# Kernel optimization log

Measured on AMD Instinct MI355X. Metric: run time of the kernel, lower is better.

## Reference

```python
import jax, jax.numpy as jnp
import numpy as np

EPS = 1e-06
SOUND_SPEED = 343.0
SUBBAND_EDGES = [500.0, 2000.0, 8000.0]
IS_SOUND_IDX = 0
RHO_IDX = 1
NUM_CANDIDATES = 64


def setup_inputs() -> dict:
    key = jax.random.key(0)
    ks = jax.random.split(key, 6)
    B, T, F, S, D = 16, 2048, 1025, 4, NUM_CANDIDATES
    phase = jax.random.normal(ks[0], (B, 1, T, F), dtype=jnp.float32)
    comb = jax.random.normal(ks[1], (B, 2, T, F), dtype=jnp.float32)
    scalar = jax.random.normal(ks[2], (B, T, S), dtype=jnp.float32)
    scalar_observed_mask = jax.random.uniform(ks[3], (B, T, S), dtype=jnp.float32)
    scalar_reliable_mask = jax.random.uniform(ks[4], (B, T, S), dtype=jnp.float32)
    stpacc = jax.random.normal(ks[5], (B, 1, T, D), dtype=jnp.float32)
    # STFT bin centers up to 24 kHz
    frequencies_hz = (jnp.arange(F, dtype=jnp.float32) * (24000.0 / (F - 1)))
    spacing_grid_hz = jnp.linspace(50.0, 1000.0, D, dtype=jnp.float32)
    return {
        'phase': phase, 'comb': comb, 'scalar': scalar,
        'scalar_observed_mask': scalar_observed_mask,
        'scalar_reliable_mask': scalar_reliable_mask,
        'stpacc': stpacc, 'frequencies_hz': frequencies_hz,
        'spacing_grid_hz': spacing_grid_hz,
    }


def _periodicity_basis(freq, spacing):
    # [D, F]: raised-cosine comb pattern for each candidate spacing
    pattern = 0.5 * (1.0 + jnp.cos(2.0 * np.pi * (freq[None, :] / jnp.maximum(spacing[:, None], 1e-06))))
    return pattern / jnp.maximum(pattern.mean(axis=-1, keepdims=True), EPS)


def _subband_masks(freq):
    # static boundaries: [min(f)] + edges + [max(f)+1]; all bands nonempty for this grid
    bounds = [jnp.min(freq)] + [jnp.float32(e) for e in SUBBAND_EDGES] + [jnp.max(freq) + 1.0]
    masks = [((freq >= lo) & (freq < hi)).astype(freq.dtype) for lo, hi in zip(bounds[:-1], bounds[1:])]
    return jnp.stack(masks, axis=0)  # [S_band, F]


def reference(phase, comb, scalar, scalar_observed_mask, scalar_reliable_mask,
              stpacc, frequencies_hz, spacing_grid_hz):
    freq = frequencies_hz.astype(phase.dtype)
    log_mag = phase[:, 0, :, :]                 # [B,T,F]
    smooth_d1 = comb[:, 0, :, :]
    abs_d1 = jnp.abs(comb[:, 1, :, :])
    log_mag_centered = log_mag - jnp.mean(log_mag, axis=-1, keepdims=True)
    trough = jax.nn.relu(-log_mag_centered)
    d1_strength = jax.nn.relu(abs_d1) + 0.25 * jax.nn.relu(jnp.abs(smooth_d1))
    trough = trough * (1.0 + d1_strength)
    trough = trough / jnp.maximum(jnp.mean(trough, axis=-1, keepdims=True), EPS)

    basis = _periodicity_basis(freq, spacing_grid_hz.astype(phase.dtype))  # [D,F]
    D, F = basis.shape
    periodic_score = jnp.einsum('btf,df->btd', trough, basis) / float(F)

    channels = [periodic_score]
    bands = _subband_masks(freq)                           # [Sb,F]
    denom = jnp.maximum(jnp.sum(bands, axis=-1), 1.0)      # [Sb]
    masked_basis = basis[None, :, :] * bands[:, None, :]   # [Sb,D,F]
    band_scores = jnp.einsum('btf,sdf->bstd', trough, masked_basis) / denom[None, :, None, None]
    channels += [band_scores[:, s] for s in range(bands.shape[0])]

    # stpacc projection (last dim already == D, no interpolation needed)
    stp = jax.nn.relu(stpacc[:, 0, :, :])
    stp = stp / jnp.maximum(jnp.mean(stp, axis=-1, keepdims=True), EPS)
    channels.append(stp)

    B, T = trough.shape[0], trough.shape[1]
    obs_quality = jnp.broadcast_to(jnp.mean(scalar_observed_mask, axis=-1, keepdims=True), (B, T, D))
    rel_quality = jnp.broadcast_to(jnp.mean(scalar_reliable_mask, axis=-1, keepdims=True), (B, T, D))
    channels.append(obs_quality)
    channels.append(rel_quality)

    is_sound = jnp.broadcast_to(jnp.clip(scalar[:, :, IS_SOUND_IDX:IS_SOUND_IDX + 1], 0.0, 1.0), (B, T, D))
    channels.append(is_sound)
    rho = jnp.broadcast_to(jnp.abs(jnp.clip(scalar[:, :, RHO_IDX:RHO_IDX + 1], -1.0, 1.0)), (B, T, D))
    channels.append(rho)

    raw_likelihood_seq = jnp.stack(channels, axis=-1)      # [B,T,D,10]
    raw_distance_logits_seq = jnp.mean(raw_likelihood_seq, axis=-1) * (0.5 + 0.5 * is_sound)

    distance_grid_cm = (100.0 * SOUND_SPEED) / (2.0 * jnp.maximum(spacing_grid_hz, 1e-06))
    return (raw_likelihood_seq, raw_distance_logits_seq,
            spacing_grid_hz.astype(phase.dtype), distance_grid_cm.astype(phase.dtype))
```

## Files before the change

### kernel.cpp

```cpp
#include <hip/hip_runtime.h>
#include <hip/hip_fp16.h>
#include <math.h>

#define Bn 16
#define Tn 2048
#define Fn 1025
#define KP 1056
#define KROW 1064
#define Dn 64
#define EPSF 1e-6f

typedef __attribute__((ext_vector_type(8))) _Float16 f16x8;
typedef __attribute__((ext_vector_type(4))) _Float16 f16x4;
typedef __attribute__((ext_vector_type(4))) float f32x4;

__device__ inline float waveReduceSum(float v) {
#pragma unroll
  for (int off = 32; off > 0; off >>= 1) v += __shfl_xor(v, off, 64);
  return v;
}

__global__ __launch_bounds__(256) void prep_kernel(
    const float* __restrict__ freq, const float* __restrict__ spacing,
    _Float16* __restrict__ basisT, float* __restrict__ out2, float* __restrict__ out3) {
  __shared__ float wsum[4];
  const int d = blockIdx.x;
  const int tid = threadIdx.x;
  const float sp = fmaxf(spacing[d], 1e-6f);

  float pv[5];
  float lsum = 0.f;
#pragma unroll
  for (int it = 0; it < 5; ++it) {
    int f = tid + 256 * it;
    float p = 0.f;
    if (f < Fn) {
      double arg = 6.2831853071795864769 * (double)(freq[f] / sp);
      p = 0.5f * (1.0f + (float)cos(arg));
      lsum += p;
    }
    pv[it] = p;
  }
  float s = waveReduceSum(lsum);
  if ((tid & 63) == 0) wsum[tid >> 6] = s;
  __syncthreads();
  float inv = 1.0f / fmaxf((wsum[0] + wsum[1] + wsum[2] + wsum[3]) * (1.0f / 1025.0f), EPSF);

#pragma unroll
  for (int it = 0; it < 5; ++it) {
    int f = tid + 256 * it;
    if (f < KP) basisT[(size_t)d * KP + f] = (_Float16)(pv[it] * inv);
  }
  if (tid == 0) {
    out2[d] = spacing[d];
    out3[d] = 17150.0f / sp;
  }
}

__global__ __launch_bounds__(256) void fused_kernel(
    const float* __restrict__ phase, const float* __restrict__ comb,
    const _Float16* __restrict__ basisT,
    const float* __restrict__ scalar, const float* __restrict__ obs_m,
    const float* __restrict__ rel_m, const float* __restrict__ stpacc,
    float* __restrict__ out0, float* __restrict__ out1) {
  __shared__ _Float16 uLDS[16 * KROW];

  const int lane = threadIdx.x & 63;
  const int w = __builtin_amdgcn_readfirstlane(threadIdx.x >> 6);
  const int row0 = blockIdx.x * 16;

#pragma unroll 1
  for (int k4 = 0; k4 < 4; ++k4) {
    const int rl = w * 4 + k4;
    const int row = row0 + rl;
    const int b = row >> 11;
    const int t = row & 2047;

    const float* prow  = phase + (size_t)row * Fn;
    const float* c0row = comb + ((size_t)(b * 2 + 0) * Tn + t) * Fn;
    const float* c1row = comb + ((size_t)(b * 2 + 1) * Tn + t) * Fn;

    float4 pv[5], c0v[5], c1v[5];
#pragma unroll
    for (int it = 0; it < 5; ++it) {
      const int i = lane + 64 * it;
      if (i < 256) {
        pv[it]  = *(const float4*)(prow  + 4 * i);
        c0v[it] = *(const float4*)(c0row + 4 * i);
        c1v[it] = *(const float4*)(c1row + 4 * i);
      } else if (i == 256) {
        pv[it]  = make_float4(prow[1024],  0.f, 0.f, 0.f);
        c0v[it] = make_float4(c0row[1024], 0.f, 0.f, 0.f);
        c1v[it] = make_float4(c1row[1024], 0.f, 0.f, 0.f);
      } else {
        pv[it]  = make_float4(0.f, 0.f, 0.f, 0.f);
        c0v[it] = make_float4(0.f, 0.f, 0.f, 0.f);
        c1v[it] = make_float4(0.f, 0.f, 0.f, 0.f);
      }
    }

    float s = 0.f;
#pragma unroll
    for (int it = 0; it < 5; ++it)
      s += pv[it].x + pv[it].y + pv[it].z + pv[it].w;
    s = waveReduceSum(s);
    const float mean_lm = s * (1.0f / 1025.0f);

    float4 uv[5];
    float su = 0.f;
#pragma unroll
    for (int it = 0; it < 5; ++it) {
      const int i = lane + 64 * it;
      float4 u;
      const float* pf = (const float*)&pv[it];
      const float* q0 = (const float*)&c0v[it];
      const float* q1 = (const float*)&c1v[it];
      float* uf = (float*)&u;
#pragma unroll
      for (int c2 = 0; c2 < 4; ++c2) {
        float tr = fmaxf(mean_lm - pf[c2], 0.f);
        float d1 = fabsf(q1[c2]) + 0.25f * fabsf(q0[c2]);
        uf[c2] = tr * (1.f + d1);
      }
      if (i > 256) { u.x = 0.f; u.y = 0.f; u.z = 0.f; u.w = 0.f; }
      else if (i == 256) { u.y = 0.f; u.z = 0.f; u.w = 0.f; }
      uv[it] = u;
      su += u.x + u.y + u.z + u.w;
    }
    su = waveReduceSum(su);
    const float rs = 1.0f / fmaxf(su * (1.0f / 1025.0f), EPSF);

    _Float16* urow = uLDS + (size_t)rl * KROW;
#pragma unroll
    for (int it = 0; it < 5; ++it) {
      const int i = lane + 64 * it;
      if (i < 264) {
        const float* uf = (const float*)&uv[it];
        f16x4 hv;
#pragma unroll
        for (int c2 = 0; c2 < 4; ++c2) hv[c2] = (_Float16)(uf[c2] * rs);
        *(f16x4*)(urow + 4 * i) = hv;
      }
    }
  }
  __syncthreads();

  const int m16 = lane & 15;
  const int kg = lane >> 4;
  const int nh = w & 1;
  const int kh = w >> 1;
  const int d0 = nh * 32 + m16;

  const _Float16* ALp = uLDS + (size_t)m16 * KROW + kg * 8;
  const _Float16* B0 = basisT + (size_t)d0 * KP + kg * 8;
  const _Float16* B1 = basisT + (size_t)(d0 + 16) * KP + kg * 8;

  f32x4 acc0 = {0.f, 0.f, 0.f, 0.f};
  f32x4 acc1 = {0.f, 0.f, 0.f, 0.f};
  f32x4 s0a = acc0, s0b = acc0, s1a = acc0, s1b = acc0, s2a = acc0, s2b = acc0;

  auto loadA = [&](int kt) { return *(const f16x8*)(ALp + kt * 32); };
  auto tileA = [&](int kt, f16x8 a) {
    f16x8 b0 = *(const f16x8*)(B0 + kt * 32);
    f16x8 b1 = *(const f16x8*)(B1 + kt * 32);
    acc0 = __builtin_amdgcn_mfma_f32_16x16x32_f16(a, b0, acc0, 0, 0, 0);
    acc1 = __builtin_amdgcn_mfma_f32_16x16x32_f16(a, b1, acc1, 0, 0, 0);
  };
  auto boundary = [&](int kt, int KB, f32x4& sa, f32x4& sb) {
    f16x8 a = loadA(kt);
    const int kb = kt * 32 + kg * 8;
    f16x8 alo, ahi;
#pragma unroll
    for (int j = 0; j < 8; ++j) {
      bool lo = (kb + j) < KB;
      alo[j] = lo ? a[j] : (_Float16)0.f;
      ahi[j] = lo ? (_Float16)0.f : a[j];
    }
    tileA(kt, alo);
    sa = acc0; sb = acc1;
    tileA(kt, ahi);
  };

  if (kh == 0) {
    boundary(0, 22, s0a, s0b);
    tileA(1, loadA(1));
    boundary(2, 86, s1a, s1b);
#pragma unroll
    for (int kt = 3; kt < 10; ++kt) tileA(kt, loadA(kt));
    boundary(10, 342, s2a, s2b);
#pragma unroll
    for (int kt = 11; kt < 16; ++kt) tileA(kt, loadA(kt));
  } else {
#pragma unroll
    for (int kt = 16; kt < 33; ++kt) tileA(kt, loadA(kt));
  }
  __syncthreads();

  float* cumL = (float*)uLDS;
  auto stor = [&](int slot, const f32x4& v0, const f32x4& v1) {
#pragma unroll
    for (int r = 0; r < 4; ++r) {
      const int rr = kg * 4 + r;
      cumL[(rr * 5 + slot) * 64 + d0]      = v0[r];
      cumL[(rr * 5 + slot) * 64 + d0 + 16] = v1[r];
    }
  };
  if (kh == 0) {
    stor(0, s0a, s0b);
    stor(1, s1a, s1b);
    stor(2, s2a, s2b);
    stor(3, acc0, acc1);
  } else {
    stor(4, acc0, acc1);
  }
  __syncthreads();

#pragma unroll
  for (int k4 = 0; k4 < 4; ++k4) {
    const int rl = w * 4 + k4;
    const size_t bt = (size_t)(row0 + rl);

    float q0 = cumL[(rl * 5 + 0) * 64 + lane];
    float q1 = cumL[(rl * 5 + 1) * 64 + lane];
    float q2 = cumL[(rl * 5 + 2) * 64 + lane];
    float q3 = cumL[(rl * 5 + 3) * 64 + lane] + cumL[(rl * 5 + 4) * 64 + lane];
    float b0 = q0, b1 = q1 - q0, b2 = q2 - q1, b3 = q3 - q2;

    float sv = fmaxf(stpacc[bt * Dn + lane], 0.f);
    float ssum = waveReduceSum(sv);
    float stp = sv / fmaxf(ssum * (1.0f / 64.0f), EPSF);

    float4 scv = *(const float4*)(scalar + bt * 4);
    float4 om  = *(const float4*)(obs_m  + bt * 4);
    float4 rm  = *(const float4*)(rel_m  + bt * 4);
    float obs_q = (om.x + om.y + om.z + om.w) * 0.25f;
    float rel_q = (rm.x + rm.y + rm.z + rm.w) * 0.25f;
    float is_snd = fminf(fmaxf(scv.x, 0.f), 1.f);
    float rho = fabsf(fminf(fmaxf(scv.y, -1.f), 1.f));

    float c0 = q3 * (1.0f / 1025.0f);
    float c1 = b0 * (1.0f / 22.0f);
    float c2 = b1 * (1.0f / 64.0f);
    float c3 = b2 * (1.0f / 256.0f);
    float c4 = b3 * (1.0f / 683.0f);

    float mean10 = (c0 + c1 + c2 + c3 + c4 + stp + obs_q + rel_q + is_snd + rho) * 0.1f;
    float logit = mean10 * (0.5f + 0.5f * is_snd);

    float2* op = (float2*)(out0 + (bt * Dn + lane) * 10);
    op[0] = make_float2(c0, c1);
    op[1] = make_float2(c2, c3);
    op[2] = make_float2(c4, stp);
    op[3] = make_float2(obs_q, rel_q);
    op[4] = make_float2(is_snd, rho);
    out1[bt * Dn + lane] = logit;
  }
}

extern "C" void kernel_launch(void* const* d_in, const int* in_sizes, int n_in,
                              void* d_out, int out_size, void* d_ws, size_t ws_size,
                              hipStream_t stream) {
  const float* phase   = (const float*)d_in[0];
  const float* comb    = (const float*)d_in[1];
  const float* scalar  = (const float*)d_in[2];
  const float* obs_m   = (const float*)d_in[3];
  const float* rel_m   = (const float*)d_in[4];
  const float* stpacc  = (const float*)d_in[5];
  const float* freq    = (const float*)d_in[6];
  const float* spacing = (const float*)d_in[7];

  float* out  = (float*)d_out;
  float* out0 = out;
  float* out1 = out + (size_t)Bn * Tn * Dn * 10;
  float* out2 = out1 + (size_t)Bn * Tn * Dn;
  float* out3 = out2 + Dn;

  _Float16* basisT = (_Float16*)d_ws;

  prep_kernel<<<Dn, 256, 0, stream>>>(freq, spacing, basisT, out2, out3);
  fused_kernel<<<Bn * Tn / 16, 256, 0, stream>>>(
      phase, comb, basisT, scalar, obs_m, rel_m, stpacc, out0, out1);
}
```

Before: 124.0 us.

## Halve rows per block and defer row normalization until after the MFMA

Each block now handles 8 rows instead of 16, which doubles the grid and halves the LDS tile to raise occupancy and latency hiding on this memory-bound kernel. The per-row normalization scale is no longer applied before the fp16 conversion. It is kept in shared memory and multiplied into the five band results after the matrix multiply, which removes a live register array and a second write pass. The cumulative-sum scratch stride is padded from 64 to 65 to reduce LDS bank conflicts. In exchange, half of each 16-row MFMA tile now computes duplicate rows, and unnormalized values stored in fp16 carry some precision and range risk.

```diff
diff --git a/kernel.cpp b/kernel.cpp
--- a/kernel.cpp
+++ b/kernel.cpp
@@ -7,6 +7,7 @@
 #define Fn 1025
 #define KP 1056
 #define KROW 1064
+#define ROWS 8
 #define Dn 64
 #define EPSF 1e-6f
 
@@ -63,15 +64,16 @@
     const float* __restrict__ scalar, const float* __restrict__ obs_m,
     const float* __restrict__ rel_m, const float* __restrict__ stpacc,
     float* __restrict__ out0, float* __restrict__ out1) {
-  __shared__ _Float16 uLDS[16 * KROW];
+  __shared__ _Float16 uLDS[ROWS * KROW];
+  __shared__ float rowScale[ROWS];
 
   const int lane = threadIdx.x & 63;
   const int w = __builtin_amdgcn_readfirstlane(threadIdx.x >> 6);
-  const int row0 = blockIdx.x * 16;
+  const int row0 = blockIdx.x * ROWS;
 
 #pragma unroll 1
-  for (int k4 = 0; k4 < 4; ++k4) {
-    const int rl = w * 4 + k4;
+  for (int k4 = 0; k4 < 2; ++k4) {
+    const int rl = w * 2 + k4;
     const int row = row0 + rl;
     const int b = row >> 11;
     const int t = row & 2047;
@@ -106,7 +108,7 @@
     s = waveReduceSum(s);
     const float mean_lm = s * (1.0f / 1025.0f);
 
-    float4 uv[5];
+    _Float16* urow = uLDS + (size_t)rl * KROW;
     float su = 0.f;
 #pragma unroll
     for (int it = 0; it < 5; ++it) {
@@ -124,24 +126,16 @@
       }
       if (i > 256) { u.x = 0.f; u.y = 0.f; u.z = 0.f; u.w = 0.f; }
       else if (i == 256) { u.y = 0.f; u.z = 0.f; u.w = 0.f; }
-      uv[it] = u;
       su += u.x + u.y + u.z + u.w;
+      if (i < 264) {
+        f16x4 hv;
+#pragma unroll
+        for (int c2 = 0; c2 < 4; ++c2) hv[c2] = (_Float16)uf[c2];
+        *(f16x4*)(urow + 4 * i) = hv;
+      }
     }
     su = waveReduceSum(su);
-    const float rs = 1.0f / fmaxf(su * (1.0f / 1025.0f), EPSF);
-
-    _Float16* urow = uLDS + (size_t)rl * KROW;
-#pragma unroll
-    for (int it = 0; it < 5; ++it) {
-      const int i = lane + 64 * it;
-      if (i < 264) {
-        const float* uf = (const float*)&uv[it];
-        f16x4 hv;
-#pragma unroll
-        for (int c2 = 0; c2 < 4; ++c2) hv[c2] = (_Float16)(uf[c2] * rs);
-        *(f16x4*)(urow + 4 * i) = hv;
-      }
-    }
+    if (lane == 0) rowScale[rl] = 1.0f / fmaxf(su * (1.0f / 1025.0f), EPSF);
   }
   __syncthreads();
 
@@ -151,7 +145,7 @@
   const int kh = w >> 1;
   const int d0 = nh * 32 + m16;
 
-  const _Float16* ALp = uLDS + (size_t)m16 * KROW + kg * 8;
+  const _Float16* ALp = uLDS + (size_t)(m16 & 7) * KROW + kg * 8;
   const _Float16* B0 = basisT + (size_t)d0 * KP + kg * 8;
   const _Float16* B1 = basisT + (size_t)(d0 + 16) * KP + kg * 8;
 
@@ -198,11 +192,13 @@
 
   float* cumL = (float*)uLDS;
   auto stor = [&](int slot, const f32x4& v0, const f32x4& v1) {
-#pragma unroll
-    for (int r = 0; r < 4; ++r) {
-      const int rr = kg * 4 + r;
-      cumL[(rr * 5 + slot) * 64 + d0]      = v0[r];
-      cumL[(rr * 5 + slot) * 64 + d0 + 16] = v1[r];
+    if (kg < 2) {
+#pragma unroll
+      for (int r = 0; r < 4; ++r) {
+        const int rr = kg * 4 + r;
+        cumL[(rr * 5 + slot) * 65 + d0]      = v0[r];
+        cumL[(rr * 5 + slot) * 65 + d0 + 16] = v1[r];
+      }
     }
   };
   if (kh == 0) {
@@ -216,14 +212,15 @@
   __syncthreads();
 
 #pragma unroll
-  for (int k4 = 0; k4 < 4; ++k4) {
-    const int rl = w * 4 + k4;
+  for (int k4 = 0; k4 < 2; ++k4) {
+    const int rl = w * 2 + k4;
     const size_t bt = (size_t)(row0 + rl);
-
-    float q0 = cumL[(rl * 5 + 0) * 64 + lane];
-    float q1 = cumL[(rl * 5 + 1) * 64 + lane];
-    float q2 = cumL[(rl * 5 + 2) * 64 + lane];
-    float q3 = cumL[(rl * 5 + 3) * 64 + lane] + cumL[(rl * 5 + 4) * 64 + lane];
+    const float rs = rowScale[rl];
+
+    float q0 = cumL[(rl * 5 + 0) * 65 + lane];
+    float q1 = cumL[(rl * 5 + 1) * 65 + lane];
+    float q2 = cumL[(rl * 5 + 2) * 65 + lane];
+    float q3 = cumL[(rl * 5 + 3) * 65 + lane] + cumL[(rl * 5 + 4) * 65 + lane];
     float b0 = q0, b1 = q1 - q0, b2 = q2 - q1, b3 = q3 - q2;
 
     float sv = fmaxf(stpacc[bt * Dn + lane], 0.f);
@@ -238,11 +235,11 @@
     float is_snd = fminf(fmaxf(scv.x, 0.f), 1.f);
     float rho = fabsf(fminf(fmaxf(scv.y, -1.f), 1.f));
 
-    float c0 = q3 * (1.0f / 1025.0f);
-    float c1 = b0 * (1.0f / 22.0f);
-    float c2 = b1 * (1.0f / 64.0f);
-    float c3 = b2 * (1.0f / 256.0f);
-    float c4 = b3 * (1.0f / 683.0f);
+    float c0 = q3 * rs * (1.0f / 1025.0f);
+    float c1 = b0 * rs * (1.0f / 22.0f);
+    float c2 = b1 * rs * (1.0f / 64.0f);
+    float c3 = b2 * rs * (1.0f / 256.0f);
+    float c4 = b3 * rs * (1.0f / 683.0f);
 
     float mean10 = (c0 + c1 + c2 + c3 + c4 + stp + obs_q + rel_q + is_snd + rho) * 0.1f;
     float logit = mean10 * (0.5f + 0.5f * is_snd);
@@ -278,6 +275,6 @@
   _Float16* basisT = (_Float16*)d_ws;
 
   prep_kernel<<<Dn, 256, 0, stream>>>(freq, spacing, basisT, out2, out3);
-  fused_kernel<<<Bn * Tn / 16, 256, 0, stream>>>(
+  fused_kernel<<<Bn * Tn / ROWS, 256, 0, stream>>>(
       phase, comb, basisT, scalar, obs_m, rel_m, stpacc, out0, out1);
 }
```

New measurement: 131.3 us. +5.9%, slower.
